# Optimization experiments

Measured on AMD Instinct MI355X. Metric: run time of the kernel, lower is better.

## Reference

```python
import jax, jax.numpy as jnp
import numpy as np

HEADS = 8
EMBED = 768
FFN = 4 * EMBED
LN_EPS = 1e-5


def _layernorm(x, g, b):
    m = jnp.mean(x, axis=-1, keepdims=True)
    v = jnp.var(x, axis=-1, keepdims=True)
    return (x - m) * jax.lax.rsqrt(v + LN_EPS) * g + b


def _attention(xn, ctx, Wq, Wkv, Wo, bo, mask):
    # xn: [B, N, C], ctx: [B, M, C], mask: [B, 1, N, M] bool (True = keep)
    B, N, C = xn.shape
    d = C // HEADS
    q = (xn @ Wq).reshape(B, N, HEADS, d).transpose(0, 2, 1, 3)          # b h i d
    k, v = jnp.split(ctx @ Wkv, 2, axis=-1)
    k = k.reshape(B, -1, HEADS, d).transpose(0, 2, 1, 3)                 # b h j d
    v = v.reshape(B, -1, HEADS, d).transpose(0, 2, 1, 3)
    sim = jnp.einsum('bhid,bhjd->bhij', q, k) * (d ** -0.5)
    sim = jnp.where(mask, sim, -jnp.finfo(sim.dtype).max)
    attn = jax.nn.softmax(sim, axis=-1)
    out = jnp.einsum('bhij,bhjd->bhid', attn, v)
    out = out.transpose(0, 2, 1, 3).reshape(B, N, C)
    return out @ Wo + bo


def _block(x, c, effect_lengths, us_rate,
           Wq1, Wkv1, Wo1, bo1, Wq2, Wkv2, Wo2, bo2,
           g1, b1, g2, b2, g4, b4, gc, bc, Wf1, bf1, Wf2, bf2):
    B, L, C = x.shape
    S = c.shape[1]
    el = effect_lengths * us_rate                                        # [B]
    i = jnp.arange(L)
    j_self = jnp.arange(L)
    j_cross = jnp.arange(S)
    # ragged per-sample masks, broadcast over heads: [B, 1, L, L] / [B, 1, L, S]
    mask1 = ((i[None, :, None] < el[:, None, None]) &
             (j_self[None, None, :] < el[:, None, None]))[:, None]
    mask2 = ((i[None, :, None] < el[:, None, None]) &
             (j_cross[None, None, :] < effect_lengths[:, None, None]))[:, None]

    xn = _layernorm(x, g1, b1)
    x = x + _attention(xn, xn, Wq1, Wkv1, Wo1, bo1, mask1)
    xn = _layernorm(x, g2, b2)
    cn = _layernorm(c, gc, bc)
    x = x + _attention(xn, cn, Wq2, Wkv2, Wo2, bo2, mask2)
    xn = _layernorm(x, g4, b4)
    x = x + (jax.nn.gelu(xn @ Wf1 + bf1, approximate=False) @ Wf2 + bf2)
    return x


def setup_inputs() -> dict:
    key = jax.random.key(0)
    ks = jax.random.split(key, 20)
    B, S, US = 8, 512, 2
    L = S * US
    s = 0.02
    inp = {
        'x': jax.random.normal(ks[0], (B, L, EMBED), jnp.float32),
        'c': jax.random.normal(ks[1], (B, S, EMBED), jnp.float32),
        'effect_lengths': jax.random.randint(ks[2], (B,), 1, S + 1),
        'us_rate': US,
        'Wq1': jax.random.normal(ks[3], (EMBED, EMBED), jnp.float32) * s,
        'Wkv1': jax.random.normal(ks[4], (EMBED, 2 * EMBED), jnp.float32) * s,
        'Wo1': jax.random.normal(ks[5], (EMBED, EMBED), jnp.float32) * s,
        'bo1': jnp.zeros((EMBED,), jnp.float32),
        'Wq2': jax.random.normal(ks[6], (EMBED, EMBED), jnp.float32) * s,
        'Wkv2': jax.random.normal(ks[7], (EMBED, 2 * EMBED), jnp.float32) * s,
        'Wo2': jax.random.normal(ks[8], (EMBED, EMBED), jnp.float32) * s,
        'bo2': jnp.zeros((EMBED,), jnp.float32),
        'g1': jnp.ones((EMBED,), jnp.float32), 'b1': jnp.zeros((EMBED,), jnp.float32),
        'g2': jnp.ones((EMBED,), jnp.float32), 'b2': jnp.zeros((EMBED,), jnp.float32),
        'g4': jnp.ones((EMBED,), jnp.float32), 'b4': jnp.zeros((EMBED,), jnp.float32),
        'gc': jnp.ones((EMBED,), jnp.float32), 'bc': jnp.zeros((EMBED,), jnp.float32),
        'Wf1': jax.random.normal(ks[9], (EMBED, FFN), jnp.float32) * s,
        'bf1': jnp.zeros((FFN,), jnp.float32),
        'Wf2': jax.random.normal(ks[10], (FFN, EMBED), jnp.float32) * s,
        'bf2': jnp.zeros((EMBED,), jnp.float32),
    }
    return inp


def reference(x, c, effect_lengths, us_rate,
              Wq1, Wkv1, Wo1, bo1, Wq2, Wkv2, Wo2, bo2,
              g1, b1, g2, b2, g4, b4, gc, bc, Wf1, bf1, Wf2, bf2):
    return _block(x, c, effect_lengths, us_rate,
                  Wq1, Wkv1, Wo1, bo1, Wq2, Wkv2, Wo2, bo2,
                  g1, b1, g2, b2, g4, b4, gc, bc, Wf1, bf1, Wf2, bf2)
```

## Files before the change

### kernel.cpp

```cpp
#include <hip/hip_runtime.h>
#include <math.h>

#define EMBED 768
#define HEADS 8
#define HDIM  96
#define NEG_MASK (-1.0e30f)

typedef unsigned short u16;
typedef unsigned int   u32;

typedef __attribute__((ext_vector_type(4))) float f32x4;
typedef __attribute__((ext_vector_type(8))) short short8;

__device__ __forceinline__ float bf2f(u16 u) {
    return __uint_as_float(((u32)u) << 16);
}
__device__ __forceinline__ u16 f2bf(float f) {
    u32 x = __float_as_uint(f);
    u32 r = (x + 0x7fffu + ((x >> 16) & 1u)) >> 16;
    return (u16)r;
}
__device__ __forceinline__ void unpack2(u32 w, float& lo, float& hi) {
    lo = __uint_as_float(w << 16);
    hi = __uint_as_float(w & 0xffff0000u);
}
__device__ __forceinline__ float wget(const void* p, size_t i, int wf) {
    return wf ? ((const float*)p)[i] : bf2f(((const u16*)p)[i]);
}
__device__ __forceinline__ int bswz(int r, int g) {
    return ((g ^ (r & 3) ^ ((r >> 2) & 3) ^ ((r >> 4) & 3)) << 3);
}

__global__ __launch_bounds__(64) void detect_kernel(const u16* __restrict__ x,
                                                    const int* __restrict__ el,
                                                    const int* __restrict__ usp,
                                                    int* __restrict__ blk) {
    int lane = threadIdx.x;
    int cnt = 0;
    for (int i = lane; i < 4096; i += 64) {
        u32 e = (x[i] >> 7) & 0xFFu;
        if (e >= 0xC0u) cnt++;
    }
#pragma unroll
    for (int off = 32; off > 0; off >>= 1) cnt += __shfl_xor(cnt, off, 64);
    if (lane == 0) {
        blk[0] = (cnt > 32) ? 1 : 0;
        bool i64 = (el[1] == 0) && (el[3] == 0) && (el[5] == 0) && (el[7] == 0);
        for (int b = 0; b < 8; b++) blk[1 + b] = i64 ? el[2 * b] : el[b];
        blk[9] = usp[0];
    }
}

__global__ void wire_to_f32(const void* __restrict__ in, size_t ioff,
                            float* __restrict__ out, int n,
                            const int* __restrict__ blk) {
    int i = blockIdx.x * blockDim.x + threadIdx.x;
    int wf = blk[0];
    if (i < n) out[i] = wget(in, ioff + (size_t)i, wf);
}
__global__ void wire_copy(const void* __restrict__ in, void* __restrict__ out,
                          int n, const int* __restrict__ blk) {
    int i = blockIdx.x * blockDim.x + threadIdx.x;
    int wf = blk[0];
    if (i < n) {
        if (wf) ((float*)out)[i] = ((const float*)in)[i];
        else    ((u16*)out)[i]   = ((const u16*)in)[i];
    }
}
__global__ void f32_to_out(const float* __restrict__ in, void* __restrict__ out,
                           size_t ooff, int n, const int* __restrict__ blk) {
    int i = blockIdx.x * blockDim.x + threadIdx.x;
    int wf = blk[0];
    if (i < n) {
        if (wf) ((float*)out)[ooff + i] = in[i];
        else    ((u16*)out)[ooff + i]   = f2bf(in[i]);
    }
}

__global__ __launch_bounds__(256) void ln_kernel(const void* __restrict__ in,
                                                 size_t ioff, int sel,
                                                 const void* __restrict__ g,
                                                 const void* __restrict__ b,
                                                 u16* __restrict__ out,
                                                 const int* __restrict__ blk) {
    int wf = blk[0];
    int row = blockIdx.x, tid = threadIdx.x;
    size_t base = ioff + (size_t)row * EMBED;
    float v[3];
#pragma unroll
    for (int e = 0; e < 3; e++) {
        size_t idx = base + tid + e * 256;
        v[e] = (sel == 0) ? ((const float*)in)[idx] : wget(in, idx, wf);
    }
    float s = v[0] + v[1] + v[2];
    float q = v[0] * v[0] + v[1] * v[1] + v[2] * v[2];
#pragma unroll
    for (int off = 32; off > 0; off >>= 1) {
        s += __shfl_xor(s, off, 64);
        q += __shfl_xor(q, off, 64);
    }
    __shared__ float sb[8];
    int wid = tid >> 6, lane = tid & 63;
    if (lane == 0) { sb[wid] = s; sb[4 + wid] = q; }
    __syncthreads();
    if (tid == 0) {
        sb[0] = sb[0] + sb[1] + sb[2] + sb[3];
        sb[4] = sb[4] + sb[5] + sb[6] + sb[7];
    }
    __syncthreads();
    float mean = sb[0] * (1.0f / EMBED);
    float var  = sb[4] * (1.0f / EMBED) - mean * mean;
    float rs   = rsqrtf(var + 1e-5f);
    size_t obase = (size_t)row * EMBED;
#pragma unroll
    for (int e = 0; e < 3; e++) {
        int col = tid + e * 256;
        out[obase + col] = f2bf((v[e] - mean) * rs * wget(g, col, wf) + wget(b, col, wf));
    }
}

__global__ __launch_bounds__(256) void gemm_kernel(const u16* __restrict__ A,
                                                   const void* __restrict__ W,
                                                   size_t woff, int ldw,
                                                   const void* __restrict__ bias, int boff,
                                                   void* __restrict__ Cv, size_t coff,
                                                   int M, int N, int K, int flags,
                                                   int tcmode, const int* __restrict__ blk) {
    __shared__ float As[16][64];
    __shared__ float Bs[16][64];
    int wf = blk[0];
    int tid = threadIdx.x;
    int tx = tid & 15, ty = tid >> 4;
    int row0 = blockIdx.y * 64, col0 = blockIdx.x * 64;
    float acc[4][4] = {};
    int ar = tid >> 2, ac4 = tid & 3;
    int br = tid >> 4, bc4 = tid & 15;

    for (int kb = 0; kb < K; kb += 16) {
        {
            uint2 u = *(const uint2*)(A + (size_t)(row0 + ar) * K + kb + ac4 * 4);
            float a0, a1, a2, a3;
            unpack2(u.x, a0, a1); unpack2(u.y, a2, a3);
            As[ac4 * 4 + 0][ar] = a0; As[ac4 * 4 + 1][ar] = a1;
            As[ac4 * 4 + 2][ar] = a2; As[ac4 * 4 + 3][ar] = a3;
        }
        {
            size_t off = woff + (size_t)(kb + br) * ldw + col0 + bc4 * 4;
            if (wf) {
                float4 u = *(const float4*)((const float*)W + off);
                Bs[br][bc4 * 4 + 0] = u.x; Bs[br][bc4 * 4 + 1] = u.y;
                Bs[br][bc4 * 4 + 2] = u.z; Bs[br][bc4 * 4 + 3] = u.w;
            } else {
                uint2 u = *(const uint2*)((const u16*)W + off);
                float b0, b1, b2, b3;
                unpack2(u.x, b0, b1); unpack2(u.y, b2, b3);
                Bs[br][bc4 * 4 + 0] = b0; Bs[br][bc4 * 4 + 1] = b1;
                Bs[br][bc4 * 4 + 2] = b2; Bs[br][bc4 * 4 + 3] = b3;
            }
        }
        __syncthreads();
#pragma unroll
        for (int kk = 0; kk < 16; kk++) {
            float4 a = *(const float4*)&As[kk][ty * 4];
            float4 b = *(const float4*)&Bs[kk][tx * 4];
            float av[4] = {a.x, a.y, a.z, a.w};
            float bv[4] = {b.x, b.y, b.z, b.w};
#pragma unroll
            for (int i = 0; i < 4; i++)
#pragma unroll
                for (int j = 0; j < 4; j++)
                    acc[i][j] += av[i] * bv[j];
        }
        __syncthreads();
    }

#pragma unroll
    for (int i = 0; i < 4; i++) {
        int m = row0 + ty * 4 + i;
#pragma unroll
        for (int j = 0; j < 4; j++) {
            int n = col0 + tx * 4 + j;
            float v = acc[i][j];
            if (flags & 1) v += wget(bias, boff + n, wf);
            if (flags & 2) v = 0.5f * v * (1.0f + erff(v * 0.70710678118654752f));
            size_t idx = coff + (size_t)m * N + n;
            if (tcmode == 0) {
                ((float*)Cv)[idx] += v;
            } else if (tcmode == 1) {
                ((u16*)Cv)[idx] = f2bf(v);
            } else {
                if (wf) ((float*)Cv)[idx] += v;
                else { u16* p = (u16*)Cv; p[idx] = f2bf(v + bf2f(p[idx])); }
            }
        }
    }
}

__global__ __launch_bounds__(256) void gemm_mfma(const u16* __restrict__ A,
                                                 const void* __restrict__ W,
                                                 size_t woff, int ldw,
                                                 const void* __restrict__ bias, int boff,
                                                 void* __restrict__ Cv, size_t coff,
                                                 int M, int N, int K, int flags,
                                                 int tcmode, const int* __restrict__ blk) {
    __shared__ __align__(16) u16 As[128 * 32];
    __shared__ __align__(16) u16 Bs[128 * 32];
    int wf = blk[0];
    int tid = threadIdx.x;
    int wave = tid >> 6, lane = tid & 63;
    int x = lane & 15, g = lane >> 4;
    int wm = wave >> 1, wn = wave & 1;
    int row0 = blockIdx.y * 128, col0 = blockIdx.x * 128;

    int ar  = tid >> 1, ah = tid & 1;
    int bk  = tid >> 3, bn0 = (tid & 7) * 16;

    f32x4 acc[4][4];
#pragma unroll
    for (int i = 0; i < 4; i++)
#pragma unroll
        for (int j = 0; j < 4; j++) acc[i][j] = (f32x4){0.f, 0.f, 0.f, 0.f};

    for (int kb = 0; kb < K; kb += 32) {
        {
            const u16* asrc = A + (size_t)(row0 + ar) * K + kb + ah * 16;
            uint4 a0 = *(const uint4*)asrc;
            uint4 a1 = *(const uint4*)(asrc + 8);
            *(uint4*)&As[ar * 32 + bswz(ar, ah * 2 + 0)] = a0;
            *(uint4*)&As[ar * 32 + bswz(ar, ah * 2 + 1)] = a1;
        }
        {
            u16 bv[16];
            if (wf) {
                const float* wsrc = (const float*)W + woff + (size_t)(kb + bk) * ldw + col0 + bn0;
#pragma unroll
                for (int i = 0; i < 16; i += 4) {
                    float4 f = *(const float4*)(wsrc + i);
                    bv[i + 0] = f2bf(f.x); bv[i + 1] = f2bf(f.y);
                    bv[i + 2] = f2bf(f.z); bv[i + 3] = f2bf(f.w);
                }
            } else {
                const u16* wsrc = (const u16*)W + woff + (size_t)(kb + bk) * ldw + col0 + bn0;
                ((uint4*)bv)[0] = *(const uint4*)wsrc;
                ((uint4*)bv)[1] = *(const uint4*)(wsrc + 8);
            }
            int kg = bk >> 3, kl = bk & 7;
#pragma unroll
            for (int i = 0; i < 16; i++)
                Bs[(bn0 + i) * 32 + bswz(bn0 + i, kg) + kl] = bv[i];
        }
        __syncthreads();

        short8 af[4], bf[4];
#pragma unroll
        for (int mt = 0; mt < 4; mt++) {
            int r = wm * 64 + mt * 16 + x;
            af[mt] = *(const short8*)&As[r * 32 + bswz(r, g)];
        }
#pragma unroll
        for (int nt = 0; nt < 4; nt++) {
            int n = wn * 64 + nt * 16 + x;
            bf[nt] = *(const short8*)&Bs[n * 32 + bswz(n, g)];
        }
#pragma unroll
        for (int mt = 0; mt < 4; mt++)
#pragma unroll
            for (int nt = 0; nt < 4; nt++)
                acc[mt][nt] = __builtin_amdgcn_mfma_f32_16x16x32_bf16(af[mt], bf[nt], acc[mt][nt], 0, 0, 0);
        __syncthreads();
    }

#pragma unroll
    for (int mt = 0; mt < 4; mt++) {
#pragma unroll
        for (int nt = 0; nt < 4; nt++) {
#pragma unroll
            for (int r = 0; r < 4; r++) {
                int m = row0 + wm * 64 + mt * 16 + g * 4 + r;
                int n = col0 + wn * 64 + nt * 16 + x;
                float v = acc[mt][nt][r];
                if (flags & 1) v += wget(bias, boff + n, wf);
                if (flags & 2) v = 0.5f * v * (1.0f + erff(v * 0.70710678118654752f));
                size_t idx = coff + (size_t)m * N + n;
                if (tcmode == 0) {
                    ((float*)Cv)[idx] += v;
                } else if (tcmode == 1) {
                    ((u16*)Cv)[idx] = f2bf(v);
                } else {
                    if (wf) ((float*)Cv)[idx] += v;
                    else { u16* p = (u16*)Cv; p[idx] = f2bf(v + bf2f(p[idx])); }
                }
            }
        }
    }
}

__global__ __launch_bounds__(256) void attn_kernel(const u16* __restrict__ Q,
                                                   const u16* __restrict__ K,
                                                   const u16* __restrict__ V,
                                                   u16* __restrict__ AO,
                                                   int ldq, int ldk, int ldv, int ldo,
                                                   size_t qss, size_t kss, size_t oss,
                                                   const int* __restrict__ blk,
                                                   int bfix, int Lk, int is_self) {
    int bz   = (bfix < 0) ? blockIdx.z : 0;
    int bidx = (bfix < 0) ? blockIdx.z : bfix;
    const u16* Qp = Q + (size_t)bz * qss;
    const u16* Kp = K + (size_t)bz * kss;
    const u16* Vp = V + (size_t)bz * kss;
    u16* AOp = AO + (size_t)bz * oss;

    int hoff = blockIdx.y * HDIM;
    int i0 = blockIdx.x * 64;
    int tid = threadIdx.x;
    int wave = tid >> 6, lane = tid & 63;
    int x = lane & 15, g = lane >> 4;

    int elb = blk[1 + bidx];
    int el_q = elb * blk[9];
    int el_k = is_self ? el_q : elb;

    __shared__ __align__(16) u16 Ks[64 * 96];
    __shared__ __align__(16) u16 Vs[96 * 64];
    __shared__ __align__(16) u16 Ps[4][16 * 72];

    short8 qf[3];
    {
        const u16* qrow = Qp + (size_t)(i0 + wave * 16 + x) * ldq + hoff;
#pragma unroll
        for (int kc = 0; kc < 3; kc++)
            qf[kc] = *(const short8*)(qrow + kc * 32 + g * 8);
    }

    const f32x4 zero4 = {0.f, 0.f, 0.f, 0.f};
    f32x4 o[6];
#pragma unroll
    for (int dt = 0; dt < 6; dt++) o[dt] = zero4;
    float m[4], l[4];
#pragma unroll
    for (int r = 0; r < 4; r++) { m[r] = NEG_MASK; l[r] = 0.f; }

    bool qok[4];
#pragma unroll
    for (int r = 0; r < 4; r++) qok[r] = (i0 + wave * 16 + g * 4 + r) < el_q;

    const float scale = 0.10206207261596576f;
    u16* pw = &Ps[wave][0];

    for (int kt0 = 0; kt0 < Lk; kt0 += 64) {
#pragma unroll
        for (int t = 0; t < 3; t++) {
            int idx = tid + t * 256;
            int j = idx / 12, c = idx % 12;
            *(uint4*)&Ks[j * 96 + c * 8] =
                *(const uint4*)(Kp + (size_t)(kt0 + j) * ldk + hoff + c * 8);
            uint4 vu = *(const uint4*)(Vp + (size_t)(kt0 + j) * ldv + hoff + c * 8);
            u16 vv[8] = {(u16)(vu.x & 0xffffu), (u16)(vu.x >> 16),
                         (u16)(vu.y & 0xffffu), (u16)(vu.y >> 16),
                         (u16)(vu.z & 0xffffu), (u16)(vu.z >> 16),
                         (u16)(vu.w & 0xffffu), (u16)(vu.w >> 16)};
            int jb = j >> 3, jl = j & 7;
#pragma unroll
            for (int ii = 0; ii < 8; ii++) {
                int d = c * 8 + ii;
                int sb = jb ^ (d & 7) ^ ((d >> 3) & 7);
                Vs[d * 64 + sb * 8 + jl] = vv[ii];
            }
        }
        __syncthreads();

        f32x4 st[4];
#pragma unroll
        for (int t = 0; t < 4; t++) {
            f32x4 acc = zero4;
#pragma unroll
            for (int kc = 0; kc < 3; kc++) {
                short8 kf = *(const short8*)&Ks[(t * 16 + x) * 96 + kc * 32 + g * 8];
                acc = __builtin_amdgcn_mfma_f32_16x16x32_bf16(qf[kc], kf, acc, 0, 0, 0);
            }
            st[t] = acc;
        }

#pragma unroll
        for (int t = 0; t < 4; t++) {
            bool kv_ok = (kt0 + t * 16 + x) < el_k;
#pragma unroll
            for (int r = 0; r < 4; r++)
                st[t][r] = (kv_ok && qok[r]) ? st[t][r] * scale : NEG_MASK;
        }

        float al[4];
#pragma unroll
        for (int r = 0; r < 4; r++) {
            float rm = fmaxf(fmaxf(st[0][r], st[1][r]), fmaxf(st[2][r], st[3][r]));
            rm = fmaxf(rm, __shfl_xor(rm, 1, 64));
            rm = fmaxf(rm, __shfl_xor(rm, 2, 64));
            rm = fmaxf(rm, __shfl_xor(rm, 4, 64));
            rm = fmaxf(rm, __shfl_xor(rm, 8, 64));
            float mn = fmaxf(m[r], rm);
            al[r] = __expf(m[r] - mn);
            m[r] = mn;
            l[r] *= al[r];
        }
#pragma unroll
        for (int dt = 0; dt < 6; dt++)
#pragma unroll
            for (int r = 0; r < 4; r++) o[dt][r] *= al[r];

#pragma unroll
        for (int t = 0; t < 4; t++)
#pragma unroll
            for (int r = 0; r < 4; r++) {
                float p = __expf(st[t][r] - m[r]);
                l[r] += p;
                pw[(g * 4 + r) * 72 + t * 16 + x] = f2bf(p);
            }

#pragma unroll
        for (int kc = 0; kc < 2; kc++) {
            short8 pf = *(const short8*)&pw[x * 72 + kc * 32 + g * 8];
#pragma unroll
            for (int dt = 0; dt < 6; dt++) {
                int d = dt * 16 + x;
                int sb = (kc * 4 + g) ^ (d & 7) ^ ((d >> 3) & 7);
                short8 vf = *(const short8*)&Vs[d * 64 + sb * 8];
                o[dt] = __builtin_amdgcn_mfma_f32_16x16x32_bf16(pf, vf, o[dt], 0, 0, 0);
            }
        }
        __syncthreads();
    }

    float inv[4];
#pragma unroll
    for (int r = 0; r < 4; r++) {
        float lr = l[r];
        lr += __shfl_xor(lr, 1, 64);
        lr += __shfl_xor(lr, 2, 64);
        lr += __shfl_xor(lr, 4, 64);
        lr += __shfl_xor(lr, 8, 64);
        inv[r] = 1.0f / lr;
    }
#pragma unroll
    for (int dt = 0; dt < 6; dt++)
#pragma unroll
        for (int r = 0; r < 4; r++) {
            size_t ob = (size_t)(i0 + wave * 16 + g * 4 + r) * ldo + hoff + dt * 16 + x;
            AOp[ob] = f2bf(o[dt][r] * inv[r]);
        }
}

extern "C" void kernel_launch(void* const* d_in, const int* in_sizes, int n_in,
                              void* d_out, int out_size, void* d_ws, size_t ws_size,
                              hipStream_t stream) {
    const void* x    = d_in[0];
    const void* c    = d_in[1];
    const int* el    = (const int*)d_in[2];
    const int* us    = (const int*)d_in[3];
    const void* Wq1  = d_in[4];
    const void* Wkv1 = d_in[5];
    const void* Wo1  = d_in[6];
    const void* bo1  = d_in[7];
    const void* Wq2  = d_in[8];
    const void* Wkv2 = d_in[9];
    const void* Wo2  = d_in[10];
    const void* bo2  = d_in[11];
    const void* g1 = d_in[12]; const void* b1 = d_in[13];
    const void* g2 = d_in[14]; const void* b2 = d_in[15];
    const void* g4 = d_in[16]; const void* b4 = d_in[17];
    const void* gc = d_in[18]; const void* bc = d_in[19];
    const void* Wf1 = d_in[20]; const void* bf1 = d_in[21];
    const void* Wf2 = d_in[22]; const void* bf2 = d_in[23];

    const int B = 8, S = 512, L = 1024, C = EMBED;
    const int NX = B * L * C;
    const size_t RL = (size_t)L * C;
    const size_t RS = (size_t)S * C;

    char* ws = (char*)d_ws;
    int*  blk = (int*)ws;
    dim3 blkd(256);

    bool tierA = ws_size >= (size_t)88080448;
    bool tierB = !tierA && ws_size >= (size_t)33030208;

    detect_kernel<<<1, 64, 0, stream>>>((const u16*)x, el, us, blk);

    if (tierA) {
        float* X  = (float*)(ws + 64);
        u16*   XN = (u16*)(ws + 64 + 25165824);
        char*  P  = ws + 64 + 25165824 + 12582912;
        u16* Qb   = (u16*)P;
        u16* KVb  = (u16*)(P + 12582912);
        u16* AOb  = (u16*)(P + 37748736);
        u16* CNb  = (u16*)P;
        u16* KV2b = (u16*)(P + 6291456);
        u16* Q2b  = (u16*)(P + 18874368);
        u16* AO2b = (u16*)(P + 31457280);
        u16* Hb   = (u16*)P;

        wire_to_f32<<<(NX + 255) / 256, blkd, 0, stream>>>(x, 0, X, NX, blk);

        ln_kernel<<<B * L, blkd, 0, stream>>>(X, 0, 0, g1, b1, XN, blk);
        gemm_mfma<<<dim3(6, 64), blkd, 0, stream>>>(XN, Wq1, 0, C, nullptr, 0, Qb, 0, B * L, C, C, 0, 1, blk);
        gemm_mfma<<<dim3(12, 64), blkd, 0, stream>>>(XN, Wkv1, 0, 2 * C, nullptr, 0, KVb, 0, B * L, 2 * C, C, 0, 1, blk);
        attn_kernel<<<dim3(16, 8, 8), blkd, 0, stream>>>(Qb, KVb, KVb + C, AOb, C, 2 * C, 2 * C, C,
                                                         RL, (size_t)L * 2 * C, RL, blk, -1, L, 1);
        gemm_mfma<<<dim3(6, 64), blkd, 0, stream>>>(AOb, Wo1, 0, C, bo1, 0, X, 0, B * L, C, C, 1, 0, blk);

        ln_kernel<<<B * L, blkd, 0, stream>>>(X, 0, 0, g2, b2, XN, blk);
        ln_kernel<<<B * S, blkd, 0, stream>>>(c, 0, 2, gc, bc, CNb, blk);
        gemm_mfma<<<dim3(12, 32), blkd, 0, stream>>>(CNb, Wkv2, 0, 2 * C, nullptr, 0, KV2b, 0, B * S, 2 * C, C, 0, 1, blk);
        gemm_mfma<<<dim3(6, 64), blkd, 0, stream>>>(XN, Wq2, 0, C, nullptr, 0, Q2b, 0, B * L, C, C, 0, 1, blk);
        attn_kernel<<<dim3(16, 8, 8), blkd, 0, stream>>>(Q2b, KV2b, KV2b + C, AO2b, C, 2 * C, 2 * C, C,
                                                         RL, (size_t)S * 2 * C, RL, blk, -1, S, 0);
        gemm_mfma<<<dim3(6, 64), blkd, 0, stream>>>(AO2b, Wo2, 0, C, bo2, 0, X, 0, B * L, C, C, 1, 0, blk);

        ln_kernel<<<B * L, blkd, 0, stream>>>(X, 0, 0, g4, b4, XN, blk);
        gemm_mfma<<<dim3(24, 64), blkd, 0, stream>>>(XN, Wf1, 0, 4 * C, bf1, 0, Hb, 0, B * L, 4 * C, C, 1 | 2, 1, blk);
        gemm_mfma<<<dim3(6, 64), blkd, 0, stream>>>(Hb, Wf2, 0, C, bf2, 0, X, 0, B * L, C, 4 * C, 1, 0, blk);

        f32_to_out<<<(NX + 255) / 256, blkd, 0, stream>>>(X, d_out, 0, NX, blk);
    } else if (tierB) {
        float* X  = (float*)(ws + 64);
        u16*   XN = (u16*)(ws + 64 + 25165824);
        char*  P  = ws + 64 + 25165824 + 1572864;
        u16* Qb   = (u16*)P;
        u16* KVb  = (u16*)(P + 1572864);
        u16* AOb  = (u16*)(P + 4718592);
        u16* CNb  = (u16*)P;
        u16* KV2b = (u16*)(P + 786432);
        u16* Q2b  = (u16*)(P + 2359296);
        u16* AO2b = (u16*)(P + 3932160);
        u16* Hb   = (u16*)P;

        wire_to_f32<<<(NX + 255) / 256, blkd, 0, stream>>>(x, 0, X, NX, blk);

        for (int b = 0; b < B; b++) {
            size_t ro = (size_t)b * RL;
            ln_kernel<<<L, blkd, 0, stream>>>(X, ro, 0, g1, b1, XN, blk);
            gemm_mfma<<<dim3(6, 8), blkd, 0, stream>>>(XN, Wq1, 0, C, nullptr, 0, Qb, 0, L, C, C, 0, 1, blk);
            gemm_mfma<<<dim3(12, 8), blkd, 0, stream>>>(XN, Wkv1, 0, 2 * C, nullptr, 0, KVb, 0, L, 2 * C, C, 0, 1, blk);
            attn_kernel<<<dim3(16, 8), blkd, 0, stream>>>(Qb, KVb, KVb + C, AOb, C, 2 * C, 2 * C, C, 0, 0, 0, blk, b, L, 1);
            gemm_mfma<<<dim3(6, 8), blkd, 0, stream>>>(AOb, Wo1, 0, C, bo1, 0, X, ro, L, C, C, 1, 0, blk);

            ln_kernel<<<L, blkd, 0, stream>>>(X, ro, 0, g2, b2, XN, blk);
            ln_kernel<<<S, blkd, 0, stream>>>(c, (size_t)b * RS, 2, gc, bc, CNb, blk);
            gemm_mfma<<<dim3(12, 4), blkd, 0, stream>>>(CNb, Wkv2, 0, 2 * C, nullptr, 0, KV2b, 0, S, 2 * C, C, 0, 1, blk);
            gemm_mfma<<<dim3(6, 8), blkd, 0, stream>>>(XN, Wq2, 0, C, nullptr, 0, Q2b, 0, L, C, C, 0, 1, blk);
            attn_kernel<<<dim3(16, 8), blkd, 0, stream>>>(Q2b, KV2b, KV2b + C, AO2b, C, 2 * C, 2 * C, C, 0, 0, 0, blk, b, S, 0);
            gemm_mfma<<<dim3(6, 8), blkd, 0, stream>>>(AO2b, Wo2, 0, C, bo2, 0, X, ro, L, C, C, 1, 0, blk);

            ln_kernel<<<L, blkd, 0, stream>>>(X, ro, 0, g4, b4, XN, blk);
            gemm_mfma<<<dim3(24, 8), blkd, 0, stream>>>(XN, Wf1, 0, 4 * C, bf1, 0, Hb, 0, L, 4 * C, C, 1 | 2, 1, blk);
            gemm_mfma<<<dim3(6, 8), blkd, 0, stream>>>(Hb, Wf2, 0, C, bf2, 0, X, ro, L, C, 4 * C, 1, 0, blk);
        }
        f32_to_out<<<(NX + 255) / 256, blkd, 0, stream>>>(X, d_out, 0, NX, blk);
    } else {
        u16*  XN  = (u16*)(ws + 64);
        u16*  CNb = (u16*)(ws + 64 + 1572864);
        char* P2  = ws + 64 + 1572864 + 786432;
        u16* Qp  = (u16*)P2;
        u16* Kp  = (u16*)(P2 + 393216);
        u16* Vp  = (u16*)(P2 + 786432);
        u16* AOp = (u16*)(P2 + 1179648);
        u16* Hc  = (u16*)P2;

        wire_copy<<<(NX + 255) / 256, blkd, 0, stream>>>(x, d_out, NX, blk);

        for (int b = 0; b < B; b++) {
            size_t ro = (size_t)b * RL;

            ln_kernel<<<L, blkd, 0, stream>>>(d_out, ro, 2, g1, b1, XN, blk);
            for (int p = 0; p < 4; p++) {
                int h = 2 * p;
                gemm_kernel<<<dim3(3, 16), blkd, 0, stream>>>(XN, Wq1, (size_t)h * 96, C, nullptr, 0, Qp, 0, L, 192, C, 0, 1, blk);
                gemm_kernel<<<dim3(3, 16), blkd, 0, stream>>>(XN, Wkv1, (size_t)h * 96, 2 * C, nullptr, 0, Kp, 0, L, 192, C, 0, 1, blk);
                gemm_kernel<<<dim3(3, 16), blkd, 0, stream>>>(XN, Wkv1, (size_t)(C + h * 96), 2 * C, nullptr, 0, Vp, 0, L, 192, C, 0, 1, blk);
                attn_kernel<<<dim3(16, 2), blkd, 0, stream>>>(Qp, Kp, Vp, AOp, 192, 192, 192, 192, 0, 0, 0, blk, b, L, 1);
                gemm_kernel<<<dim3(12, 16), blkd, 0, stream>>>(AOp, Wo1, (size_t)h * 96 * C, C, bo1, 0, d_out, ro, L, C, 192, (p == 0) ? 1 : 0, 3, blk);
            }
            ln_kernel<<<L, blkd, 0, stream>>>(d_out, ro, 2, g2, b2, XN, blk);
            ln_kernel<<<S, blkd, 0, stream>>>(c, (size_t)b * RS, 2, gc, bc, CNb, blk);
            for (int p = 0; p < 4; p++) {
                int h = 2 * p;
                gemm_kernel<<<dim3(3, 16), blkd, 0, stream>>>(XN, Wq2, (size_t)h * 96, C, nullptr, 0, Qp, 0, L, 192, C, 0, 1, blk);
                gemm_kernel<<<dim3(3, 8), blkd, 0, stream>>>(CNb, Wkv2, (size_t)h * 96, 2 * C, nullptr, 0, Kp, 0, S, 192, C, 0, 1, blk);
                gemm_kernel<<<dim3(3, 8), blkd, 0, stream>>>(CNb, Wkv2, (size_t)(C + h * 96), 2 * C, nullptr, 0, Vp, 0, S, 192, C, 0, 1, blk);
                attn_kernel<<<dim3(16, 2), blkd, 0, stream>>>(Qp, Kp, Vp, AOp, 192, 192, 192, 192, 0, 0, 0, blk, b, S, 0);
                gemm_kernel<<<dim3(12, 16), blkd, 0, stream>>>(AOp, Wo2, (size_t)h * 96 * C, C, bo2, 0, d_out, ro, L, C, 192, (p == 0) ? 1 : 0, 3, blk);
            }
            ln_kernel<<<L, blkd, 0, stream>>>(d_out, ro, 2, g4, b4, XN, blk);
            for (int ch = 0; ch < 4; ch++) {
                gemm_kernel<<<dim3(12, 16), blkd, 0, stream>>>(XN, Wf1, (size_t)ch * C, 4 * C, bf1, ch * C, Hc, 0, L, C, C, 1 | 2, 1, blk);
                gemm_kernel<<<dim3(12, 16), blkd, 0, stream>>>(Hc, Wf2, (size_t)ch * C * C, C, bf2, 0, d_out, ro, L, C, C, (ch == 0) ? 1 : 0, 3, blk);
            }
        }
    }
}
```

Measured before the change: 939.3 us.

## Pre-transpose weights to bf16 and use double-buffered transposed-B MFMA GEMM

Adds a kernel that converts each weight matrix to a transposed bf16 copy in workspace, plus a new GEMM that reads the transposed B with contiguous 16-byte loads and double-buffers its LDS tiles so the next K-slice loads while MFMAs run. The tier-A path switches all GEMMs to this kernel. Attention output is written back into the Q buffer to save workspace, and the FFN is split into two row halves so the hidden buffer fits beside the new weight buffer. The cost is extra transpose launches each call and twice the FFN launches.

```diff
diff --git a/kernel.cpp b/kernel.cpp
--- a/kernel.cpp
+++ b/kernel.cpp
@@ -74,6 +74,40 @@
     if (i < n) {
         if (wf) ((float*)out)[ooff + i] = in[i];
         else    ((u16*)out)[ooff + i]   = f2bf(in[i]);
+    }
+}
+
+__global__ __launch_bounds__(256) void wtrans_kernel(const void* __restrict__ W, size_t woff,
+                                                     int ldw, int K,
+                                                     u16* __restrict__ WT,
+                                                     const int* __restrict__ blk) {
+    __shared__ u16 T[64][65];
+    int wf = blk[0];
+    int n0 = blockIdx.x * 64, k0 = blockIdx.y * 64;
+    int tid = threadIdx.x;
+    int tr = tid >> 4, tc4 = (tid & 15) * 4;
+#pragma unroll
+    for (int i = 0; i < 4; i++) {
+        int k = tr + i * 16;
+        if (wf) {
+            const float* src = (const float*)W + woff + (size_t)(k0 + k) * ldw + n0 + tc4;
+            float4 f = *(const float4*)src;
+            T[tc4 + 0][k] = f2bf(f.x); T[tc4 + 1][k] = f2bf(f.y);
+            T[tc4 + 2][k] = f2bf(f.z); T[tc4 + 3][k] = f2bf(f.w);
+        } else {
+            const u16* src = (const u16*)W + woff + (size_t)(k0 + k) * ldw + n0 + tc4;
+            uint2 u = *(const uint2*)src;
+            T[tc4 + 0][k] = (u16)(u.x & 0xffffu); T[tc4 + 1][k] = (u16)(u.x >> 16);
+            T[tc4 + 2][k] = (u16)(u.y & 0xffffu); T[tc4 + 3][k] = (u16)(u.y >> 16);
+        }
+    }
+    __syncthreads();
+#pragma unroll
+    for (int i = 0; i < 4; i++) {
+        int n = tr + i * 16;
+        u32 w0 = (u32)T[n][tc4 + 0] | ((u32)T[n][tc4 + 1] << 16);
+        u32 w1 = (u32)T[n][tc4 + 2] | ((u32)T[n][tc4 + 3] << 16);
+        *(uint2*)(WT + (size_t)(n0 + n) * K + k0 + tc4) = make_uint2(w0, w1);
     }
 }
 
@@ -268,6 +302,112 @@
             for (int nt = 0; nt < 4; nt++)
                 acc[mt][nt] = __builtin_amdgcn_mfma_f32_16x16x32_bf16(af[mt], bf[nt], acc[mt][nt], 0, 0, 0);
         __syncthreads();
+    }
+
+#pragma unroll
+    for (int mt = 0; mt < 4; mt++) {
+#pragma unroll
+        for (int nt = 0; nt < 4; nt++) {
+#pragma unroll
+            for (int r = 0; r < 4; r++) {
+                int m = row0 + wm * 64 + mt * 16 + g * 4 + r;
+                int n = col0 + wn * 64 + nt * 16 + x;
+                float v = acc[mt][nt][r];
+                if (flags & 1) v += wget(bias, boff + n, wf);
+                if (flags & 2) v = 0.5f * v * (1.0f + erff(v * 0.70710678118654752f));
+                size_t idx = coff + (size_t)m * N + n;
+                if (tcmode == 0) {
+                    ((float*)Cv)[idx] += v;
+                } else if (tcmode == 1) {
+                    ((u16*)Cv)[idx] = f2bf(v);
+                } else {
+                    if (wf) ((float*)Cv)[idx] += v;
+                    else { u16* p = (u16*)Cv; p[idx] = f2bf(v + bf2f(p[idx])); }
+                }
+            }
+        }
+    }
+}
+
+__global__ __launch_bounds__(256) void gemm_mfma_t(const u16* __restrict__ A,
+                                                   const u16* __restrict__ BT,
+                                                   const void* __restrict__ bias, int boff,
+                                                   void* __restrict__ Cv, size_t coff,
+                                                   int M, int N, int K, int flags,
+                                                   int tcmode, const int* __restrict__ blk) {
+    __shared__ __align__(16) u16 As[2][128 * 32];
+    __shared__ __align__(16) u16 Bs[2][128 * 32];
+    int wf = blk[0];
+    int tid = threadIdx.x;
+    int wave = tid >> 6, lane = tid & 63;
+    int x = lane & 15, g = lane >> 4;
+    int wm = wave >> 1, wn = wave & 1;
+    int row0 = blockIdx.y * 128, col0 = blockIdx.x * 128;
+
+    int sr = tid >> 1;
+    int sg = (tid & 1) * 2;
+    const u16* aptr = A  + (size_t)(row0 + sr) * K + sg * 8;
+    const u16* bptr = BT + (size_t)(col0 + sr) * K + sg * 8;
+    int wo0 = sr * 32 + bswz(sr, sg);
+    int wo1 = sr * 32 + bswz(sr, sg + 1);
+
+    int ra[4], rb[4];
+#pragma unroll
+    for (int t = 0; t < 4; t++) {
+        int r = wm * 64 + t * 16 + x;
+        int n = wn * 64 + t * 16 + x;
+        ra[t] = r * 32 + bswz(r, g);
+        rb[t] = n * 32 + bswz(n, g);
+    }
+
+    f32x4 acc[4][4];
+#pragma unroll
+    for (int i = 0; i < 4; i++)
+#pragma unroll
+        for (int j = 0; j < 4; j++) acc[i][j] = (f32x4){0.f, 0.f, 0.f, 0.f};
+
+    {
+        uint4 a0 = *(const uint4*)aptr, a1 = *(const uint4*)(aptr + 8);
+        uint4 b0 = *(const uint4*)bptr, b1 = *(const uint4*)(bptr + 8);
+        *(uint4*)&As[0][wo0] = a0; *(uint4*)&As[0][wo1] = a1;
+        *(uint4*)&Bs[0][wo0] = b0; *(uint4*)&Bs[0][wo1] = b1;
+    }
+    __syncthreads();
+
+    int nsteps = K >> 5;
+    int cur = 0;
+    for (int s = 0; s < nsteps - 1; ++s) {
+        aptr += 32; bptr += 32;
+        uint4 pa0 = *(const uint4*)aptr, pa1 = *(const uint4*)(aptr + 8);
+        uint4 pb0 = *(const uint4*)bptr, pb1 = *(const uint4*)(bptr + 8);
+
+        short8 af[4], bfr[4];
+#pragma unroll
+        for (int mt = 0; mt < 4; mt++) af[mt] = *(const short8*)&As[cur][ra[mt]];
+#pragma unroll
+        for (int nt = 0; nt < 4; nt++) bfr[nt] = *(const short8*)&Bs[cur][rb[nt]];
+#pragma unroll
+        for (int mt = 0; mt < 4; mt++)
+#pragma unroll
+            for (int nt = 0; nt < 4; nt++)
+                acc[mt][nt] = __builtin_amdgcn_mfma_f32_16x16x32_bf16(af[mt], bfr[nt], acc[mt][nt], 0, 0, 0);
+
+        *(uint4*)&As[cur ^ 1][wo0] = pa0; *(uint4*)&As[cur ^ 1][wo1] = pa1;
+        *(uint4*)&Bs[cur ^ 1][wo0] = pb0; *(uint4*)&Bs[cur ^ 1][wo1] = pb1;
+        __syncthreads();
+        cur ^= 1;
+    }
+    {
+        short8 af[4], bfr[4];
+#pragma unroll
+        for (int mt = 0; mt < 4; mt++) af[mt] = *(const short8*)&As[cur][ra[mt]];
+#pragma unroll
+        for (int nt = 0; nt < 4; nt++) bfr[nt] = *(const short8*)&Bs[cur][rb[nt]];
+#pragma unroll
+        for (int mt = 0; mt < 4; mt++)
+#pragma unroll
+            for (int nt = 0; nt < 4; nt++)
+                acc[mt][nt] = __builtin_amdgcn_mfma_f32_16x16x32_bf16(af[mt], bfr[nt], acc[mt][nt], 0, 0, 0);
     }
 
 #pragma unroll
@@ -487,37 +627,52 @@
 
     if (tierA) {
         float* X  = (float*)(ws + 64);
-        u16*   XN = (u16*)(ws + 64 + 25165824);
-        char*  P  = ws + 64 + 25165824 + 12582912;
+        u16*   XN = (u16*)(ws + 25165888);
+        u16*   WT = (u16*)(ws + 37748800);
+        char*  P  = ws + 47185984;
         u16* Qb   = (u16*)P;
         u16* KVb  = (u16*)(P + 12582912);
-        u16* AOb  = (u16*)(P + 37748736);
         u16* CNb  = (u16*)P;
         u16* KV2b = (u16*)(P + 6291456);
         u16* Q2b  = (u16*)(P + 18874368);
-        u16* AO2b = (u16*)(P + 31457280);
-        u16* Hb   = (u16*)P;
+        u16* Hh   = (u16*)P;
+        const size_t WTq = 0, WTkv = 589824, WTo = 1769472;
+        const size_t WTf1 = 0, WTf2 = 2359296;
 
         wire_to_f32<<<(NX + 255) / 256, blkd, 0, stream>>>(x, 0, X, NX, blk);
 
+        wtrans_kernel<<<dim3(12, 12), blkd, 0, stream>>>(Wq1, 0, C, C, WT + WTq, blk);
+        wtrans_kernel<<<dim3(24, 12), blkd, 0, stream>>>(Wkv1, 0, 2 * C, C, WT + WTkv, blk);
+        wtrans_kernel<<<dim3(12, 12), blkd, 0, stream>>>(Wo1, 0, C, C, WT + WTo, blk);
+
         ln_kernel<<<B * L, blkd, 0, stream>>>(X, 0, 0, g1, b1, XN, blk);
-        gemm_mfma<<<dim3(6, 64), blkd, 0, stream>>>(XN, Wq1, 0, C, nullptr, 0, Qb, 0, B * L, C, C, 0, 1, blk);
-        gemm_mfma<<<dim3(12, 64), blkd, 0, stream>>>(XN, Wkv1, 0, 2 * C, nullptr, 0, KVb, 0, B * L, 2 * C, C, 0, 1, blk);
-        attn_kernel<<<dim3(16, 8, 8), blkd, 0, stream>>>(Qb, KVb, KVb + C, AOb, C, 2 * C, 2 * C, C,
+        gemm_mfma_t<<<dim3(6, 64), blkd, 0, stream>>>(XN, WT + WTq, nullptr, 0, Qb, 0, B * L, C, C, 0, 1, blk);
+        gemm_mfma_t<<<dim3(12, 64), blkd, 0, stream>>>(XN, WT + WTkv, nullptr, 0, KVb, 0, B * L, 2 * C, C, 0, 1, blk);
+        attn_kernel<<<dim3(16, 8, 8), blkd, 0, stream>>>(Qb, KVb, KVb + C, Qb, C, 2 * C, 2 * C, C,
                                                          RL, (size_t)L * 2 * C, RL, blk, -1, L, 1);
-        gemm_mfma<<<dim3(6, 64), blkd, 0, stream>>>(AOb, Wo1, 0, C, bo1, 0, X, 0, B * L, C, C, 1, 0, blk);
+        gemm_mfma_t<<<dim3(6, 64), blkd, 0, stream>>>(Qb, WT + WTo, bo1, 0, X, 0, B * L, C, C, 1, 0, blk);
+
+        wtrans_kernel<<<dim3(12, 12), blkd, 0, stream>>>(Wq2, 0, C, C, WT + WTq, blk);
+        wtrans_kernel<<<dim3(24, 12), blkd, 0, stream>>>(Wkv2, 0, 2 * C, C, WT + WTkv, blk);
+        wtrans_kernel<<<dim3(12, 12), blkd, 0, stream>>>(Wo2, 0, C, C, WT + WTo, blk);
 
         ln_kernel<<<B * L, blkd, 0, stream>>>(X, 0, 0, g2, b2, XN, blk);
         ln_kernel<<<B * S, blkd, 0, stream>>>(c, 0, 2, gc, bc, CNb, blk);
-        gemm_mfma<<<dim3(12, 32), blkd, 0, stream>>>(CNb, Wkv2, 0, 2 * C, nullptr, 0, KV2b, 0, B * S, 2 * C, C, 0, 1, blk);
-        gemm_mfma<<<dim3(6, 64), blkd, 0, stream>>>(XN, Wq2, 0, C, nullptr, 0, Q2b, 0, B * L, C, C, 0, 1, blk);
-        attn_kernel<<<dim3(16, 8, 8), blkd, 0, stream>>>(Q2b, KV2b, KV2b + C, AO2b, C, 2 * C, 2 * C, C,
+        gemm_mfma_t<<<dim3(12, 32), blkd, 0, stream>>>(CNb, WT + WTkv, nullptr, 0, KV2b, 0, B * S, 2 * C, C, 0, 1, blk);
+        gemm_mfma_t<<<dim3(6, 64), blkd, 0, stream>>>(XN, WT + WTq, nullptr, 0, Q2b, 0, B * L, C, C, 0, 1, blk);
+        attn_kernel<<<dim3(16, 8, 8), blkd, 0, stream>>>(Q2b, KV2b, KV2b + C, Q2b, C, 2 * C, 2 * C, C,
                                                          RL, (size_t)S * 2 * C, RL, blk, -1, S, 0);
-        gemm_mfma<<<dim3(6, 64), blkd, 0, stream>>>(AO2b, Wo2, 0, C, bo2, 0, X, 0, B * L, C, C, 1, 0, blk);
+        gemm_mfma_t<<<dim3(6, 64), blkd, 0, stream>>>(Q2b, WT + WTo, bo2, 0, X, 0, B * L, C, C, 1, 0, blk);
+
+        wtrans_kernel<<<dim3(48, 12), blkd, 0, stream>>>(Wf1, 0, 4 * C, C, WT + WTf1, blk);
+        wtrans_kernel<<<dim3(12, 48), blkd, 0, stream>>>(Wf2, 0, C, 4 * C, WT + WTf2, blk);
 
         ln_kernel<<<B * L, blkd, 0, stream>>>(X, 0, 0, g4, b4, XN, blk);
-        gemm_mfma<<<dim3(24, 64), blkd, 0, stream>>>(XN, Wf1, 0, 4 * C, bf1, 0, Hb, 0, B * L, 4 * C, C, 1 | 2, 1, blk);
-        gemm_mfma<<<dim3(6, 64), blkd, 0, stream>>>(Hb, Wf2, 0, C, bf2, 0, X, 0, B * L, C, 4 * C, 1, 0, blk);
+        for (int h = 0; h < 2; h++) {
+            size_t ro = (size_t)h * 4096 * C;
+            gemm_mfma_t<<<dim3(24, 32), blkd, 0, stream>>>(XN + ro, WT + WTf1, bf1, 0, Hh, 0, 4096, 4 * C, C, 1 | 2, 1, blk);
+            gemm_mfma_t<<<dim3(6, 32), blkd, 0, stream>>>(Hh, WT + WTf2, bf2, 0, X, ro, 4096, C, 4 * C, 1, 0, blk);
+        }
 
         f32_to_out<<<(NX + 255) / 256, blkd, 0, stream>>>(X, d_out, 0, NX, blk);
     } else if (tierB) {
```

Result: faster. 895.4 us (-4.7%).
